# Kernel optimization log

Measured on AMD Instinct MI355X. Metric: run time of the kernel, lower is better.

Reference implementation:

```python
import jax, jax.numpy as jnp
import numpy as np

N, C_BANDS, D_MODEL, D_STATE = 4096, 224, 64, 16
LN_EPS = 1e-5


def setup_inputs() -> dict:
    key = jax.random.key(0)
    ks = jax.random.split(key, 9)
    g = lambda k, shape, scale: jax.random.normal(k, shape, dtype=jnp.float32) * scale
    return {
        "x": g(ks[0], (N, C_BANDS), 1.0),
        # input_proj: Linear(1, d_model) -> weight (d_model,1) flattened + bias
        "w_in": g(ks[1], (D_MODEL,), 1.0),
        "b_in": g(ks[2], (D_MODEL,), 0.1),
        "A_log": g(ks[3], (D_MODEL, D_STATE), 0.1),
        # B_proj / C_proj: Linear(d_model, d_state, bias=False); stored as (d_model, d_state)
        "Wb": g(ks[4], (D_MODEL, D_STATE), 1.0 / np.sqrt(D_MODEL)),
        "Wc": g(ks[5], (D_MODEL, D_STATE), 1.0 / np.sqrt(D_MODEL)),
        "D": jnp.ones((D_MODEL,), jnp.float32),
        # out_proj: Linear(d_model, d_model), torch convention weight (out,in)
        "Wo": g(ks[6], (D_MODEL, D_MODEL), 1.0 / np.sqrt(D_MODEL)),
        "bo": g(ks[7], (D_MODEL,), 0.1),
        "gamma": jnp.ones((D_MODEL,), jnp.float32),
        "beta": jnp.zeros((D_MODEL,), jnp.float32),
    }


def reference(x, w_in, b_in, A_log, Wb, Wc, D, Wo, bo, gamma, beta):
    # x: (N, C) -> x_emb: (N, C, d_model) via Linear(1, d_model)
    x_emb = x[:, :, None] * w_in + b_in
    A_exp = jnp.exp(-jnp.exp(A_log))                      # (d, s), fixed decay
    # selective B/C projections for every band, computed vectorized
    Bseq = jnp.einsum('ncd,ds->cns', x_emb, Wb)           # (C, N, s)
    Cseq = jnp.einsum('ncd,ds->cns', x_emb, Wc)           # (C, N, s)
    useq = jnp.transpose(x_emb, (1, 0, 2))                # (C, N, d)

    h0 = jnp.zeros((x.shape[0], D_MODEL, D_STATE), x.dtype)

    def step(h, inp):
        u, Bk = inp
        h = h * A_exp + u[:, :, None] * Bk[:, None, :]    # (N, d, s)
        return h, None

    h_final, _ = jax.lax.scan(step, h0, (useq, Bseq))
    # y in the torch loop is overwritten each step; only the last readout matters
    y = jnp.einsum('nds,ns->nd', h_final, Cseq[-1])       # (N, d)

    out = y + D * x_emb[:, -1, :]
    z = out @ Wo.T + bo
    mu = jnp.mean(z, axis=-1, keepdims=True)
    var = jnp.mean((z - mu) ** 2, axis=-1, keepdims=True)
    return gamma * (z - mu) * jax.lax.rsqrt(var + LN_EPS) + beta
```

## Files before the change

### kernel.cpp

```cpp
#include <hip/hip_runtime.h>

#define N_SAMPLES 4096
#define C_BANDS   224
#define D_MODEL   64
#define D_STATE   16
#define KTAIL     20
#define LN_EPS    1e-5f

#define WS_G 0
#define WS_U (KTAIL * 64 * 4)

__global__ __launch_bounds__(256) void ssm_setup(
    const float* __restrict__ w_in, const float* __restrict__ b_in,
    const float* __restrict__ A_log, const float* __restrict__ Wb,
    const float* __restrict__ Wc, const float* __restrict__ Dvec,
    const float* __restrict__ Wo, const float* __restrict__ bo,
    float* __restrict__ ws)
{
    __shared__ float eAL[D_MODEL * D_STATE];
    __shared__ float ppL[64];
    __shared__ float qL[4][16];
    __shared__ float TpL[4][4][D_MODEL];
    __shared__ float coefL[4][D_MODEL];
    __shared__ float gpL[4][4][D_MODEL];

    const int t = threadIdx.x;
    const int k = blockIdx.x;

    {
        const float4 v = *(const float4*)(A_log + 4 * t);
        eAL[4*t+0] = __expf(v.x); eAL[4*t+1] = __expf(v.y);
        eAL[4*t+2] = __expf(v.z); eAL[4*t+3] = __expf(v.w);
    }
    if (t < 64) {
        const int s = t & 15, which = t >> 4;
        const float* vin = (which & 1) ? b_in : w_in;
        const float* wm  = (which & 2) ? Wc : Wb;
        float p = 0.f;
        #pragma unroll 8
        for (int dd = 0; dd < D_MODEL; ++dd)
            p = fmaf(vin[dd], wm[dd * D_STATE + s], p);
        ppL[t] = p;
    }
    __syncthreads();
    if (t < 16) {
        const float wb = ppL[t], bb = ppL[16+t], wc = ppL[32+t], bc = ppL[48+t];
        qL[0][t] = wc * wb; qL[1][t] = wc * bb;
        qL[2][t] = bc * wb; qL[3][t] = bc * bb;
    }
    __syncthreads();

    const int d    = t & 63;
    const int part = t >> 6;
    float t1 = 0.f, t2 = 0.f, t3 = 0.f, t4 = 0.f;
    if (k < KTAIL) {
        const float e = (float)(KTAIL - 1 - k);
        #pragma unroll
        for (int j = 0; j < 4; ++j) {
            const int s = 4 * part + j;
            const float w = __expf(-e * eAL[d * D_STATE + s]);
            t1 = fmaf(qL[0][s], w, t1);
            t2 = fmaf(qL[1][s], w, t2);
            t3 = fmaf(qL[2][s], w, t3);
            t4 = fmaf(qL[3][s], w, t4);
        }
    } else {
        #pragma unroll
        for (int j = 0; j < 4; ++j) {
            const int s = 4 * part + j;
            const float a  = __expf(-eAL[d * D_STATE + s]);
            const float s0 = __builtin_amdgcn_rcpf(1.f - a);
            t2 = fmaf(qL[1][s], s0, t2);
            t4 = fmaf(qL[3][s], s0, t4);
        }
    }
    TpL[part][0][d] = t1; TpL[part][1][d] = t2;
    TpL[part][2][d] = t3; TpL[part][3][d] = t4;
    __syncthreads();

    if (t < 64) {
        const float T1 = TpL[0][0][d]+TpL[1][0][d]+TpL[2][0][d]+TpL[3][0][d];
        const float T2 = TpL[0][1][d]+TpL[1][1][d]+TpL[2][1][d]+TpL[3][1][d];
        const float T3 = TpL[0][2][d]+TpL[1][2][d]+TpL[2][2][d]+TpL[3][2][d];
        const float T4 = TpL[0][3][d]+TpL[1][3][d]+TpL[2][3][d]+TpL[3][3][d];
        const float wi = w_in[d], bi = b_in[d];
        if (k < KTAIL) {
            coefL[0][d] = wi * T1;
            coefL[1][d] = fmaf(wi, T2, bi * T1);
            coefL[2][d] = wi * T3;
            coefL[3][d] = fmaf(wi, T4, bi * T3);
        } else {
            const float dv = Dvec[d];
            coefL[0][d] = fmaf(dv, wi, bi * T2);
            coefL[1][d] = fmaf(dv, bi, bi * T4);
            coefL[2][d] = 0.f;
            coefL[3][d] = 0.f;
        }
    }
    __syncthreads();

    const int o = t & 63, q = t >> 6;
    float g1 = 0.f, g2 = 0.f, g3 = 0.f, g4 = 0.f;
    const float4* wo4 = (const float4*)(Wo + o * D_MODEL + 16 * q);
    #pragma unroll
    for (int jj = 0; jj < 4; ++jj) {
        const float4 w4 = wo4[jj];
        const int d0 = 16 * q + 4 * jj;
        #define FOLD(i2, WV)                                  \
        {   g1 = fmaf(coefL[0][d0 + i2], WV, g1);             \
            g2 = fmaf(coefL[1][d0 + i2], WV, g2);             \
            g3 = fmaf(coefL[2][d0 + i2], WV, g3);             \
            g4 = fmaf(coefL[3][d0 + i2], WV, g4); }
        FOLD(0, w4.x) FOLD(1, w4.y) FOLD(2, w4.z) FOLD(3, w4.w)
        #undef FOLD
    }
    gpL[q][0][o] = g1; gpL[q][1][o] = g2; gpL[q][2][o] = g3; gpL[q][3][o] = g4;
    __syncthreads();

    if (t < 64) {
        const float G1 = gpL[0][0][o]+gpL[1][0][o]+gpL[2][0][o]+gpL[3][0][o];
        const float G2 = gpL[0][1][o]+gpL[1][1][o]+gpL[2][1][o]+gpL[3][1][o];
        const float G3 = gpL[0][2][o]+gpL[1][2][o]+gpL[2][2][o]+gpL[3][2][o];
        const float G4 = gpL[0][3][o]+gpL[1][3][o]+gpL[2][3][o]+gpL[3][3][o];
        if (k < KTAIL)
            ((float4*)(ws + WS_G))[k * 64 + o] = make_float4(G1, G2, G3, G4);
        else
            ((float2*)(ws + WS_U))[o] = make_float2(G1, G2 + bo[o]);
    }
}

__global__ __launch_bounds__(256) void ssm_main(
    const float* __restrict__ x,
    const float* __restrict__ gamma,
    const float* __restrict__ beta,
    const float* __restrict__ ws,
    float* __restrict__ out)
{
    const int tid  = threadIdx.x;
    const int wave = tid >> 6;
    const int lane = tid & 63;
    const int n    = __builtin_amdgcn_readfirstlane(blockIdx.x * 4 + wave);

    float xt[KTAIL];
    {
        const float4* xp = (const float4*)(x + n * C_BANDS + (C_BANDS - KTAIL));
        #pragma unroll
        for (int qd = 0; qd < KTAIL / 4; ++qd) {
            const float4 v = xp[qd];
            xt[4*qd+0] = v.x; xt[4*qd+1] = v.y; xt[4*qd+2] = v.z; xt[4*qd+3] = v.w;
        }
    }

    const float2 u = ((const float2*)(ws + WS_U))[lane];
    const float4* G = (const float4*)(ws + WS_G);
    float A = 0.f, B = 0.f, Cc = 0.f, Dd = 0.f;
    #pragma unroll
    for (int k = 0; k < KTAIL; ++k) {
        const float4 g  = G[k * 64 + lane];
        const float xk  = xt[k];
        const float x2k = xk * xk;
        A  = fmaf(x2k, g.x, A);
        B  = fmaf(xk,  g.y, B);
        Cc = fmaf(x2k, g.z, Cc);
        Dd = fmaf(xk,  g.w, Dd);
    }
    const float x_last = xt[KTAIL - 1];
    const float z = fmaf(x_last, (A + B) + u.x, (Cc + Dd) + u.y);

    float ssum = z;
    #pragma unroll
    for (int off = 32; off > 0; off >>= 1) ssum += __shfl_xor(ssum, off, 64);
    const float mu = ssum * (1.f / 64.f);
    const float zd = z - mu;
    float vs = zd * zd;
    #pragma unroll
    for (int off = 32; off > 0; off >>= 1) vs += __shfl_xor(vs, off, 64);
    const float inv = rsqrtf(vs * (1.f / 64.f) + LN_EPS);
    out[n * D_MODEL + lane] = fmaf(gamma[lane] * zd, inv, beta[lane]);
}

extern "C" void kernel_launch(void* const* d_in, const int* in_sizes, int n_in,
                              void* d_out, int out_size, void* d_ws, size_t ws_size,
                              hipStream_t stream) {
    const float* x     = (const float*)d_in[0];
    const float* w_in  = (const float*)d_in[1];
    const float* b_in  = (const float*)d_in[2];
    const float* A_log = (const float*)d_in[3];
    const float* Wb    = (const float*)d_in[4];
    const float* Wc    = (const float*)d_in[5];
    const float* Dvec  = (const float*)d_in[6];
    const float* Wo    = (const float*)d_in[7];
    const float* bo    = (const float*)d_in[8];
    const float* gamma = (const float*)d_in[9];
    const float* beta  = (const float*)d_in[10];
    float* out = (float*)d_out;
    float* ws  = (float*)d_ws;

    ssm_setup<<<KTAIL + 1, 256, 0, stream>>>(
        w_in, b_in, A_log, Wb, Wc, Dvec, Wo, bo, ws);
    ssm_main<<<N_SAMPLES / 4, 256, 0, stream>>>(x, gamma, beta, ws, out);
}
```

Measured before the change: 14.05 us.

## Fuse setup and main kernels, recomputing folded weights per block in LDS

Merges the weight-folding setup kernel into the main kernel. Each 1024-thread block now recomputes the full table of per-row coefficients (21 rows by 64) in shared memory, then processes 16 samples from it. This drops the second kernel launch and the workspace round trip through global memory. In exchange, every one of the 256 blocks repeats the exp-heavy setup and a 64x64 fold against Wo, and the larger blocks may lower occupancy.

```diff
diff --git a/kernel.cpp b/kernel.cpp
--- a/kernel.cpp
+++ b/kernel.cpp
@@ -5,33 +5,28 @@
 #define D_MODEL   64
 #define D_STATE   16
 #define KTAIL     20
+#define NROWS     (KTAIL + 1)
 #define LN_EPS    1e-5f
 
-#define WS_G 0
-#define WS_U (KTAIL * 64 * 4)
-
-__global__ __launch_bounds__(256) void ssm_setup(
+__global__ __launch_bounds__(1024) void ssm_all(
+    const float* __restrict__ x,
     const float* __restrict__ w_in, const float* __restrict__ b_in,
     const float* __restrict__ A_log, const float* __restrict__ Wb,
     const float* __restrict__ Wc, const float* __restrict__ Dvec,
     const float* __restrict__ Wo, const float* __restrict__ bo,
-    float* __restrict__ ws)
+    const float* __restrict__ gamma, const float* __restrict__ beta,
+    float* __restrict__ out)
 {
-    __shared__ float eAL[D_MODEL * D_STATE];
-    __shared__ float ppL[64];
-    __shared__ float qL[4][16];
-    __shared__ float TpL[4][4][D_MODEL];
-    __shared__ float coefL[4][D_MODEL];
-    __shared__ float gpL[4][4][D_MODEL];
+    __shared__ float  eAL[D_MODEL * D_STATE];
+    __shared__ float  ppL[64];
+    __shared__ float  qL[4][16];
+    __shared__ float4 coefL[NROWS][D_MODEL];
+    __shared__ float4 GL[NROWS * D_MODEL];
 
     const int t = threadIdx.x;
-    const int k = blockIdx.x;
 
-    {
-        const float4 v = *(const float4*)(A_log + 4 * t);
-        eAL[4*t+0] = __expf(v.x); eAL[4*t+1] = __expf(v.y);
-        eAL[4*t+2] = __expf(v.z); eAL[4*t+3] = __expf(v.w);
-    }
+    eAL[t] = __expf(A_log[t]);
+
     if (t < 64) {
         const int s = t & 15, which = t >> 4;
         const float* vin = (which & 1) ? b_in : w_in;
@@ -50,96 +45,66 @@
     }
     __syncthreads();
 
-    const int d    = t & 63;
-    const int part = t >> 6;
-    float t1 = 0.f, t2 = 0.f, t3 = 0.f, t4 = 0.f;
-    if (k < KTAIL) {
-        const float e = (float)(KTAIL - 1 - k);
-        #pragma unroll
-        for (int j = 0; j < 4; ++j) {
-            const int s = 4 * part + j;
-            const float w = __expf(-e * eAL[d * D_STATE + s]);
-            t1 = fmaf(qL[0][s], w, t1);
-            t2 = fmaf(qL[1][s], w, t2);
-            t3 = fmaf(qL[2][s], w, t3);
-            t4 = fmaf(qL[3][s], w, t4);
-        }
-    } else {
-        #pragma unroll
-        for (int j = 0; j < 4; ++j) {
-            const int s = 4 * part + j;
-            const float a  = __expf(-eAL[d * D_STATE + s]);
-            const float s0 = __builtin_amdgcn_rcpf(1.f - a);
-            t2 = fmaf(qL[1][s], s0, t2);
-            t4 = fmaf(qL[3][s], s0, t4);
-        }
-    }
-    TpL[part][0][d] = t1; TpL[part][1][d] = t2;
-    TpL[part][2][d] = t3; TpL[part][3][d] = t4;
-    __syncthreads();
-
-    if (t < 64) {
-        const float T1 = TpL[0][0][d]+TpL[1][0][d]+TpL[2][0][d]+TpL[3][0][d];
-        const float T2 = TpL[0][1][d]+TpL[1][1][d]+TpL[2][1][d]+TpL[3][1][d];
-        const float T3 = TpL[0][2][d]+TpL[1][2][d]+TpL[2][2][d]+TpL[3][2][d];
-        const float T4 = TpL[0][3][d]+TpL[1][3][d]+TpL[2][3][d]+TpL[3][3][d];
+    for (int e0 = t; e0 < NROWS * D_MODEL; e0 += 1024) {
+        const int r = e0 >> 6, d = e0 & 63;
         const float wi = w_in[d], bi = b_in[d];
-        if (k < KTAIL) {
-            coefL[0][d] = wi * T1;
-            coefL[1][d] = fmaf(wi, T2, bi * T1);
-            coefL[2][d] = wi * T3;
-            coefL[3][d] = fmaf(wi, T4, bi * T3);
+        if (r < KTAIL) {
+            const float e = (float)(KTAIL - 1 - r);
+            float t1 = 0.f, t2 = 0.f, t3 = 0.f, t4 = 0.f;
+            #pragma unroll
+            for (int s = 0; s < D_STATE; ++s) {
+                const float w = __expf(-e * eAL[d * D_STATE + s]);
+                t1 = fmaf(qL[0][s], w, t1);
+                t2 = fmaf(qL[1][s], w, t2);
+                t3 = fmaf(qL[2][s], w, t3);
+                t4 = fmaf(qL[3][s], w, t4);
+            }
+            coefL[r][d] = make_float4(wi * t1,
+                                      fmaf(wi, t2, bi * t1),
+                                      wi * t3,
+                                      fmaf(wi, t4, bi * t3));
         } else {
+            float t2 = 0.f, t4 = 0.f;
+            #pragma unroll
+            for (int s = 0; s < D_STATE; ++s) {
+                const float a  = __expf(-eAL[d * D_STATE + s]);
+                const float s0 = __builtin_amdgcn_rcpf(1.f - a);
+                t2 = fmaf(qL[1][s], s0, t2);
+                t4 = fmaf(qL[3][s], s0, t4);
+            }
             const float dv = Dvec[d];
-            coefL[0][d] = fmaf(dv, wi, bi * T2);
-            coefL[1][d] = fmaf(dv, bi, bi * T4);
-            coefL[2][d] = 0.f;
-            coefL[3][d] = 0.f;
+            coefL[r][d] = make_float4(fmaf(dv, wi, bi * t2),
+                                      fmaf(dv, bi, bi * t4),
+                                      0.f, 0.f);
         }
     }
     __syncthreads();
 
-    const int o = t & 63, q = t >> 6;
-    float g1 = 0.f, g2 = 0.f, g3 = 0.f, g4 = 0.f;
-    const float4* wo4 = (const float4*)(Wo + o * D_MODEL + 16 * q);
-    #pragma unroll
-    for (int jj = 0; jj < 4; ++jj) {
-        const float4 w4 = wo4[jj];
-        const int d0 = 16 * q + 4 * jj;
-        #define FOLD(i2, WV)                                  \
-        {   g1 = fmaf(coefL[0][d0 + i2], WV, g1);             \
-            g2 = fmaf(coefL[1][d0 + i2], WV, g2);             \
-            g3 = fmaf(coefL[2][d0 + i2], WV, g3);             \
-            g4 = fmaf(coefL[3][d0 + i2], WV, g4); }
-        FOLD(0, w4.x) FOLD(1, w4.y) FOLD(2, w4.z) FOLD(3, w4.w)
-        #undef FOLD
+    for (int e0 = t; e0 < NROWS * D_MODEL; e0 += 1024) {
+        const int r = e0 >> 6, o = e0 & 63;
+        float g1 = 0.f, g2 = 0.f, g3 = 0.f, g4 = 0.f;
+        const float4* wo4 = (const float4*)(Wo + o * D_MODEL);
+        #pragma unroll 4
+        for (int dq = 0; dq < D_MODEL / 4; ++dq) {
+            const float4 w4 = wo4[dq];
+            const int d0 = 4 * dq;
+            #define FOLD(i2, WV)                                  \
+            {   const float4 c = coefL[r][d0 + i2];               \
+                g1 = fmaf(c.x, WV, g1);                           \
+                g2 = fmaf(c.y, WV, g2);                           \
+                g3 = fmaf(c.z, WV, g3);                           \
+                g4 = fmaf(c.w, WV, g4); }
+            FOLD(0, w4.x) FOLD(1, w4.y) FOLD(2, w4.z) FOLD(3, w4.w)
+            #undef FOLD
+        }
+        if (r == KTAIL) g2 += bo[o];
+        GL[e0] = make_float4(g1, g2, g3, g4);
     }
-    gpL[q][0][o] = g1; gpL[q][1][o] = g2; gpL[q][2][o] = g3; gpL[q][3][o] = g4;
     __syncthreads();
 
-    if (t < 64) {
-        const float G1 = gpL[0][0][o]+gpL[1][0][o]+gpL[2][0][o]+gpL[3][0][o];
-        const float G2 = gpL[0][1][o]+gpL[1][1][o]+gpL[2][1][o]+gpL[3][1][o];
-        const float G3 = gpL[0][2][o]+gpL[1][2][o]+gpL[2][2][o]+gpL[3][2][o];
-        const float G4 = gpL[0][3][o]+gpL[1][3][o]+gpL[2][3][o]+gpL[3][3][o];
-        if (k < KTAIL)
-            ((float4*)(ws + WS_G))[k * 64 + o] = make_float4(G1, G2, G3, G4);
-        else
-            ((float2*)(ws + WS_U))[o] = make_float2(G1, G2 + bo[o]);
-    }
-}
-
-__global__ __launch_bounds__(256) void ssm_main(
-    const float* __restrict__ x,
-    const float* __restrict__ gamma,
-    const float* __restrict__ beta,
-    const float* __restrict__ ws,
-    float* __restrict__ out)
-{
-    const int tid  = threadIdx.x;
-    const int wave = tid >> 6;
-    const int lane = tid & 63;
-    const int n    = __builtin_amdgcn_readfirstlane(blockIdx.x * 4 + wave);
+    const int wave = t >> 6;
+    const int lane = t & 63;
+    const int n    = __builtin_amdgcn_readfirstlane(blockIdx.x * 16 + wave);
 
     float xt[KTAIL];
     {
@@ -151,12 +116,11 @@
         }
     }
 
-    const float2 u = ((const float2*)(ws + WS_U))[lane];
-    const float4* G = (const float4*)(ws + WS_G);
+    const float4 u4 = GL[KTAIL * D_MODEL + lane];
     float A = 0.f, B = 0.f, Cc = 0.f, Dd = 0.f;
     #pragma unroll
     for (int k = 0; k < KTAIL; ++k) {
-        const float4 g  = G[k * 64 + lane];
+        const float4 g  = GL[k * D_MODEL + lane];
         const float xk  = xt[k];
         const float x2k = xk * xk;
         A  = fmaf(x2k, g.x, A);
@@ -165,7 +129,7 @@
         Dd = fmaf(xk,  g.w, Dd);
     }
     const float x_last = xt[KTAIL - 1];
-    const float z = fmaf(x_last, (A + B) + u.x, (Cc + Dd) + u.y);
+    const float z = fmaf(x_last, (A + B) + u4.x, (Cc + Dd) + u4.y);
 
     float ssum = z;
     #pragma unroll
@@ -194,9 +158,7 @@
     const float* gamma = (const float*)d_in[9];
     const float* beta  = (const float*)d_in[10];
     float* out = (float*)d_out;
-    float* ws  = (float*)d_ws;
 
-    ssm_setup<<<KTAIL + 1, 256, 0, stream>>>(
-        w_in, b_in, A_log, Wb, Wc, Dvec, Wo, bo, ws);
-    ssm_main<<<N_SAMPLES / 4, 256, 0, stream>>>(x, gamma, beta, ws, out);
+    ssm_all<<<N_SAMPLES / 16, 1024, 0, stream>>>(
+        x, w_in, b_in, A_log, Wb, Wc, Dvec, Wo, bo, gamma, beta, out);
 }
```

Result: slower. 22.43 us (+59.7%).
